# Optimization experiments

Hardware: AMD Instinct MI355X
Metric: run time of the kernel (lower is better)

Reference implementation:

```python
import jax, jax.numpy as jnp
import numpy as np

N_NODES = 100000
D_IN, D_OUT = 1024, 512
B, K = 8192, 64


def setup_inputs() -> dict:
    key = jax.random.key(0)
    k1, k2, k3, k4, k5 = jax.random.split(key, 5)
    X = jax.random.normal(k1, (N_NODES, D_IN), dtype=jnp.float32)
    indices = jax.random.randint(k2, (B, K), 0, N_NODES)  # top-K PPR neighbor ids per batch node
    values = jax.random.uniform(k3, (B, K), dtype=jnp.float32)  # PPR weights
    W = jax.random.normal(k4, (D_IN, D_OUT), dtype=jnp.float32) / np.sqrt(D_IN)
    b = jax.random.normal(k5, (D_OUT,), dtype=jnp.float32)
    return {"X": X, "indices": indices, "values": values, "W": W, "b": b}


def reference(X, indices, values, W, b):
    # Sparse PPR branch. Original: encode only unique gathered rows, then
    # re-expand via inverse indices. Since the encoder is row-pointwise,
    # encoder(X[u_fwd])[u_bwd] == encoder(X)[indices]; we encode all nodes once
    # (n_nodes < B*K here) then gather -- identical math, jit-friendly.
    enc = X @ W + b                      # [N, d_out]
    gathered = enc[indices]              # [B, K, d_out]
    return jnp.einsum('bk,bkd->bd', values, gathered)  # weighted sum over K neighbors
```

## Files before the change

### kernel.cpp

```cpp
#include <hip/hip_runtime.h>

typedef unsigned short ushort_t;
typedef __bf16 bf16x8 __attribute__((ext_vector_type(8)));
typedef float f32x4 __attribute__((ext_vector_type(4)));

#define N_NODES 100000
#define M_PAD   100096
#define D_IN    1024
#define D_OUT   512
#define B_SZ    8192
#define K_NB    64

__device__ __forceinline__ ushort_t f2bf(float f) {
    unsigned int u = __builtin_bit_cast(unsigned int, f);
    u += 0x7FFFu + ((u >> 16) & 1u);
    return (ushort_t)(u >> 16);
}
__device__ __forceinline__ float bflo(unsigned d) {
    return __builtin_bit_cast(float, d << 16);
}
__device__ __forceinline__ float bfhi(unsigned d) {
    return __builtin_bit_cast(float, d & 0xFFFF0000u);
}

__device__ __forceinline__ void gload16(const ushort_t* g, ushort_t* l) {
    __builtin_amdgcn_global_load_lds(
        (const __attribute__((address_space(1))) void*)g,
        (__attribute__((address_space(3))) void*)l,
        16, 0, 0);
}

__device__ __forceinline__ bf16x8 pack8(float4 a, float4 b) {
    bf16x8 r;
    r[0] = (__bf16)a.x; r[1] = (__bf16)a.y;
    r[2] = (__bf16)a.z; r[3] = (__bf16)a.w;
    r[4] = (__bf16)b.x; r[5] = (__bf16)b.y;
    r[6] = (__bf16)b.z; r[7] = (__bf16)b.w;
    return r;
}

__global__ __launch_bounds__(256) void cast_w_kernel(
        const float* __restrict__ W, ushort_t* __restrict__ Wt) {
    int o = blockIdx.x * 256 + threadIdx.x;
    int n = o >> 10;
    int k = o & 1023;
    Wt[o] = f2bf(W[k * D_OUT + n]);
}

__global__ __launch_bounds__(256) void encode_gemm_kernel(
        const float* __restrict__ X, const ushort_t* __restrict__ Wt,
        const float* __restrict__ bias, ushort_t* __restrict__ Enc) {
    int bid = blockIdx.x;
    int logical = (bid & 7) * 391 + (bid >> 3);
    int m0 = (logical >> 2) * 128;
    int n0 = (logical & 3) * 128;

    int tid = threadIdx.x;
    int lane = tid & 63;
    int wave = tid >> 6;
    int wm = (wave >> 1) * 64;
    int wn = (wave & 1) * 64;
    int quad = lane >> 4;
    int l16  = lane & 15;

    __shared__ __align__(16) ushort_t As[2 * 4096];
    __shared__ __align__(16) ushort_t Bs[2 * 4096];

    f32x4 acc[4][4];
    f32x4 zero = {0.f, 0.f, 0.f, 0.f};
    #pragma unroll
    for (int i = 0; i < 4; i++)
        #pragma unroll
        for (int j = 0; j < 4; j++)
            acc[i][j] = zero;

    int srow = tid >> 2;
    int kch  = tid & 3;
    int schk = kch ^ ((srow >> 2) & 3);

    const ushort_t* gb = Wt + (size_t)(n0 + srow) * D_IN + schk * 8;
    ushort_t* lb = Bs + tid * 8;
    const size_t rowskip = (size_t)64 * D_IN;

    int ar0 = m0 + srow;
    int ar1 = m0 + srow + 64;
    if (ar0 > N_NODES - 1) ar0 = N_NODES - 1;
    if (ar1 > N_NODES - 1) ar1 = N_NODES - 1;
    const float* pa0 = X + (size_t)ar0 * D_IN + kch * 8;
    const float* pa1 = X + (size_t)ar1 * D_IN + kch * 8;
    ushort_t* aw = As + srow * 32 + schk * 8;

    int rsw  = (l16 >> 2) & 3;
    int rchk = quad ^ rsw;

    {
        float4 f00 = *(const float4*)(pa0);
        float4 f01 = *(const float4*)(pa0 + 4);
        float4 f10 = *(const float4*)(pa1);
        float4 f11 = *(const float4*)(pa1 + 4);
        gload16(gb,           lb);
        gload16(gb + rowskip, lb + 2048);
        *(bf16x8*)(aw)           = pack8(f00, f01);
        *(bf16x8*)(aw + 64 * 32) = pack8(f10, f11);
    }
    __syncthreads();

    for (int it = 0; it < 32; ++it) {
        int p  = (it & 1) * 4096;
        int q  = 4096 - p;
        int k1 = it * 32 + 32;

        float4 g00, g01, g10, g11;
        bool has_next = (k1 < D_IN);
        if (has_next) {
            g00 = *(const float4*)(pa0 + k1);
            g01 = *(const float4*)(pa0 + k1 + 4);
            g10 = *(const float4*)(pa1 + k1);
            g11 = *(const float4*)(pa1 + k1 + 4);
            gload16(gb + k1,           lb + q);
            gload16(gb + rowskip + k1, lb + q + 2048);
        }

        bf16x8 a[4], b[4];
        #pragma unroll
        for (int i = 0; i < 4; i++) {
            a[i] = *(const bf16x8*)(As + p + (wm + i * 16 + l16) * 32 + rchk * 8);
            b[i] = *(const bf16x8*)(Bs + p + (wn + i * 16 + l16) * 32 + rchk * 8);
        }
        #pragma unroll
        for (int i = 0; i < 4; i++)
            #pragma unroll
            for (int j = 0; j < 4; j++)
                acc[i][j] = __builtin_amdgcn_mfma_f32_16x16x32_bf16(
                                a[i], b[j], acc[i][j], 0, 0, 0);

        if (has_next) {
            *(bf16x8*)(aw + q)           = pack8(g00, g01);
            *(bf16x8*)(aw + q + 64 * 32) = pack8(g10, g11);
        }
        __syncthreads();
    }

    float bv[4];
    #pragma unroll
    for (int j = 0; j < 4; j++) bv[j] = bias[n0 + wn + j * 16 + l16];

    #pragma unroll
    for (int i = 0; i < 4; i++) {
        #pragma unroll
        for (int r = 0; r < 4; r++) {
            int grow = m0 + wm + i * 16 + quad * 4 + r;
            if (grow < N_NODES) {
                #pragma unroll
                for (int j = 0; j < 4; j++) {
                    int gcol = n0 + wn + j * 16 + l16;
                    Enc[(size_t)grow * D_OUT + gcol] = f2bf(acc[i][j][r] + bv[j]);
                }
            }
        }
    }
}

__global__ __launch_bounds__(256) void gather_out_kernel(
        const ushort_t* __restrict__ Enc, const int* __restrict__ idx,
        const float* __restrict__ val, float* __restrict__ out) {
    int b = blockIdx.x;
    int t = threadIdx.x;

    __shared__ int   sidx[K_NB];
    __shared__ float sval[K_NB];
    __shared__ float part[8 * 3 * 64];
    if (t < K_NB) {
        sidx[t] = idx[b * K_NB + t];
        sval[t] = val[b * K_NB + t];
    }
    __syncthreads();

    int h = t >> 6;
    int c = t & 63;

    float acc[8] = {0.f, 0.f, 0.f, 0.f, 0.f, 0.f, 0.f, 0.f};

    uint4 x[8];
    #pragma unroll
    for (int u = 0; u < 8; u++)
        x[u] = ((const uint4*)(Enc + (size_t)sidx[h + 4 * u] * D_OUT))[c];

    #pragma unroll
    for (int j0 = 0; j0 < 16; j0 += 8) {
        uint4 cur[8];
        #pragma unroll
        for (int u = 0; u < 8; u++) cur[u] = x[u];
        if (j0 + 8 < 16) {
            #pragma unroll
            for (int u = 0; u < 8; u++)
                x[u] = ((const uint4*)(
                    Enc + (size_t)sidx[h + 4 * (j0 + 8 + u)] * D_OUT))[c];
        }
        #pragma unroll
        for (int u = 0; u < 8; u++) {
            float v = sval[h + 4 * (j0 + u)];
            acc[0] = fmaf(v, bflo(cur[u].x), acc[0]);
            acc[1] = fmaf(v, bfhi(cur[u].x), acc[1]);
            acc[2] = fmaf(v, bflo(cur[u].y), acc[2]);
            acc[3] = fmaf(v, bfhi(cur[u].y), acc[3]);
            acc[4] = fmaf(v, bflo(cur[u].z), acc[4]);
            acc[5] = fmaf(v, bfhi(cur[u].z), acc[5]);
            acc[6] = fmaf(v, bflo(cur[u].w), acc[6]);
            acc[7] = fmaf(v, bfhi(cur[u].w), acc[7]);
        }
    }

    if (h != 0) {
        #pragma unroll
        for (int e = 0; e < 8; e++)
            part[e * 192 + (h - 1) * 64 + c] = acc[e];
    }
    __syncthreads();
    if (h == 0) {
        float r[8];
        #pragma unroll
        for (int e = 0; e < 8; e++)
            r[e] = acc[e] + part[e * 192 + c] + part[e * 192 + 64 + c]
                          + part[e * 192 + 128 + c];
        float4 o0 = {r[0], r[1], r[2], r[3]};
        float4 o1 = {r[4], r[5], r[6], r[7]};
        float* dst = out + (size_t)b * D_OUT + c * 8;
        *(float4*)(dst)     = o0;
        *(float4*)(dst + 4) = o1;
    }
}

__global__ __launch_bounds__(256) void gather_f32_kernel(
        const float* __restrict__ X, const int* __restrict__ idx,
        const float* __restrict__ val, ushort_t* __restrict__ Y,
        float* __restrict__ s) {
    int b = blockIdx.x;
    int t = threadIdx.x;

    __shared__ int   sidx[K_NB];
    __shared__ float sval[K_NB];
    if (t < K_NB) {
        sidx[t] = idx[b * K_NB + t];
        sval[t] = val[b * K_NB + t];
    }
    __syncthreads();

    float ax = 0.f, ay = 0.f, az = 0.f, aw = 0.f;
    #pragma unroll 8
    for (int k = 0; k < K_NB; k++) {
        const float4* row = (const float4*)(X + (size_t)sidx[k] * D_IN);
        float4 x = row[t];
        float  v = sval[k];
        ax = fmaf(v, x.x, ax);
        ay = fmaf(v, x.y, ay);
        az = fmaf(v, x.z, az);
        aw = fmaf(v, x.w, aw);
    }
    uint2 o;
    o.x = (unsigned)f2bf(ax) | ((unsigned)f2bf(ay) << 16);
    o.y = (unsigned)f2bf(az) | ((unsigned)f2bf(aw) << 16);
    *(uint2*)(Y + (size_t)b * D_IN + t * 4) = o;

    if (t == 0) {
        float sum = 0.f;
        #pragma unroll
        for (int k = 0; k < K_NB; k++) sum += sval[k];
        s[b] = sum;
    }
}

__global__ __launch_bounds__(256) void gemm_kernel(
        const ushort_t* __restrict__ Y, const ushort_t* __restrict__ Wt,
        const float* __restrict__ s, const float* __restrict__ bias,
        float* __restrict__ out) {
    const int Kdim = D_IN;
    int m0 = blockIdx.x * 128;
    int n0 = blockIdx.y * 128;
    int t = threadIdx.x;
    int lane = t & 63;
    int wave = t >> 6;
    int wm = (wave >> 1) * 64;
    int wn = (wave & 1) * 64;
    int quad = lane >> 4;
    int l16  = lane & 15;

    __shared__ __align__(16) ushort_t As[128 * 32];
    __shared__ __align__(16) ushort_t Bs[128 * 32];

    f32x4 acc[4][4];
    f32x4 zero = {0.f, 0.f, 0.f, 0.f};
    #pragma unroll
    for (int i = 0; i < 4; i++)
        #pragma unroll
        for (int j = 0; j < 4; j++)
            acc[i][j] = zero;

    int rsw = (l16 >> 2) & 3;

    for (int k0 = 0; k0 < Kdim; k0 += 32) {
        #pragma unroll
        for (int i = 0; i < 2; i++) {
            int c   = t + i * 256;
            int row = c >> 2;
            int chk = c & 3;
            int pos = chk ^ ((row >> 2) & 3);
            *(int4*)(As + row * 32 + pos * 8) =
                *(const int4*)(Y + (size_t)(m0 + row) * Kdim + k0 + chk * 8);
            *(int4*)(Bs + row * 32 + pos * 8) =
                *(const int4*)(Wt + (size_t)(n0 + row) * Kdim + k0 + chk * 8);
        }
        __syncthreads();

        bf16x8 a[4], b[4];
        int rchk = quad ^ rsw;
        #pragma unroll
        for (int i = 0; i < 4; i++) {
            a[i] = *(const bf16x8*)(As + (wm + i * 16 + l16) * 32 + rchk * 8);
            b[i] = *(const bf16x8*)(Bs + (wn + i * 16 + l16) * 32 + rchk * 8);
        }
        #pragma unroll
        for (int i = 0; i < 4; i++)
            #pragma unroll
            for (int j = 0; j < 4; j++)
                acc[i][j] = __builtin_amdgcn_mfma_f32_16x16x32_bf16(
                                a[i], b[j], acc[i][j], 0, 0, 0);
        __syncthreads();
    }

    #pragma unroll
    for (int i = 0; i < 4; i++) {
        #pragma unroll
        for (int r = 0; r < 4; r++) {
            int grow = m0 + wm + i * 16 + quad * 4 + r;
            float sv = s[grow];
            #pragma unroll
            for (int j = 0; j < 4; j++) {
                int gcol = n0 + wn + j * 16 + l16;
                out[(size_t)grow * D_OUT + gcol] = acc[i][j][r] + sv * bias[gcol];
            }
        }
    }
}

extern "C" void kernel_launch(void* const* d_in, const int* in_sizes, int n_in,
                              void* d_out, int out_size, void* d_ws, size_t ws_size,
                              hipStream_t stream) {
    const float* X    = (const float*)d_in[0];
    const int*   idx  = (const int*)d_in[1];
    const float* val  = (const float*)d_in[2];
    const float* W    = (const float*)d_in[3];
    const float* bias = (const float*)d_in[4];
    float* out = (float*)d_out;

    const size_t ENC_BYTES = (size_t)M_PAD * D_OUT * 2;
    const size_t WT_BYTES  = (size_t)D_OUT * D_IN * 2;
    const size_t Y_BYTES   = (size_t)B_SZ * D_IN * 2;

    char* ws = (char*)d_ws;
    bool fast = ws_size >= ENC_BYTES + WT_BYTES;

    if (fast) {
        ushort_t* Enc = (ushort_t*)ws;
        ushort_t* Wt  = (ushort_t*)(ws + ENC_BYTES);

        hipLaunchKernelGGL(cast_w_kernel, dim3((D_OUT * D_IN) / 256), dim3(256),
                           0, stream, W, Wt);
        hipLaunchKernelGGL(encode_gemm_kernel, dim3((M_PAD / 128) * (D_OUT / 128)),
                           dim3(256), 0, stream, X, Wt, bias, Enc);
        hipLaunchKernelGGL(gather_out_kernel, dim3(B_SZ), dim3(256),
                           0, stream, Enc, idx, val, out);
    } else {
        ushort_t* Yb = (ushort_t*)ws;
        ushort_t* Wt = (ushort_t*)(ws + Y_BYTES);
        float*    sb = (float*)(ws + Y_BYTES + WT_BYTES);

        hipLaunchKernelGGL(cast_w_kernel, dim3((D_OUT * D_IN) / 256), dim3(256),
                           0, stream, W, Wt);
        hipLaunchKernelGGL(gather_f32_kernel, dim3(B_SZ), dim3(256),
                           0, stream, X, idx, val, Yb, sb);
        hipLaunchKernelGGL(gemm_kernel, dim3(B_SZ / 128, D_OUT / 128), dim3(256),
                           0, stream, Yb, Wt, sb, bias, out);
    }
}
```

Before: 783.9 us.

## Use single-buffered 64-wide K tiles with register prefetch in encode GEMM

The encode GEMM now steps through K in tiles of 64 instead of 32. It drops the LDS double buffer and uses one 128x64 tile per operand with an 8-chunk XOR swizzle. The next X tile is prefetched into registers while the MFMAs run on the current one. This halves the number of loop iterations and barriers and gives each barrier interval more MFMA work. The cost is that the W async loads are no longer overlapped with compute, since there are two barriers per iteration on a single buffer.

```diff
diff --git a/kernel.cpp b/kernel.cpp
--- a/kernel.cpp
+++ b/kernel.cpp
@@ -63,8 +63,8 @@
     int quad = lane >> 4;
     int l16  = lane & 15;
 
-    __shared__ __align__(16) ushort_t As[2 * 4096];
-    __shared__ __align__(16) ushort_t Bs[2 * 4096];
+    __shared__ __align__(16) ushort_t As[128 * 64];
+    __shared__ __align__(16) ushort_t Bs[128 * 64];
 
     f32x4 acc[4][4];
     f32x4 zero = {0.f, 0.f, 0.f, 0.f};
@@ -74,69 +74,63 @@
         for (int j = 0; j < 4; j++)
             acc[i][j] = zero;
 
-    int srow = tid >> 2;
-    int kch  = tid & 3;
-    int schk = kch ^ ((srow >> 2) & 3);
-
-    const ushort_t* gb = Wt + (size_t)(n0 + srow) * D_IN + schk * 8;
+    int rb  = tid >> 3;
+    int kc  = tid & 7;
+    int skc = kc ^ (rb & 7);
+
+    const ushort_t* gb = Wt + (size_t)(n0 + rb) * D_IN + skc * 8;
     ushort_t* lb = Bs + tid * 8;
-    const size_t rowskip = (size_t)64 * D_IN;
-
-    int ar0 = m0 + srow;
-    int ar1 = m0 + srow + 64;
-    if (ar0 > N_NODES - 1) ar0 = N_NODES - 1;
-    if (ar1 > N_NODES - 1) ar1 = N_NODES - 1;
-    const float* pa0 = X + (size_t)ar0 * D_IN + kch * 8;
-    const float* pa1 = X + (size_t)ar1 * D_IN + kch * 8;
-    ushort_t* aw = As + srow * 32 + schk * 8;
-
-    int rsw  = (l16 >> 2) & 3;
-    int rchk = quad ^ rsw;
-
-    {
-        float4 f00 = *(const float4*)(pa0);
-        float4 f01 = *(const float4*)(pa0 + 4);
-        float4 f10 = *(const float4*)(pa1);
-        float4 f11 = *(const float4*)(pa1 + 4);
-        gload16(gb,           lb);
-        gload16(gb + rowskip, lb + 2048);
-        *(bf16x8*)(aw)           = pack8(f00, f01);
-        *(bf16x8*)(aw + 64 * 32) = pack8(f10, f11);
-    }
-    __syncthreads();
-
-    for (int it = 0; it < 32; ++it) {
-        int p  = (it & 1) * 4096;
-        int q  = 4096 - p;
-        int k1 = it * 32 + 32;
-
-        float4 g00, g01, g10, g11;
-        bool has_next = (k1 < D_IN);
-        if (has_next) {
-            g00 = *(const float4*)(pa0 + k1);
-            g01 = *(const float4*)(pa0 + k1 + 4);
-            g10 = *(const float4*)(pa1 + k1);
-            g11 = *(const float4*)(pa1 + k1 + 4);
-            gload16(gb + k1,           lb + q);
-            gload16(gb + rowskip + k1, lb + q + 2048);
-        }
-
-        bf16x8 a[4], b[4];
-        #pragma unroll
-        for (int i = 0; i < 4; i++) {
-            a[i] = *(const bf16x8*)(As + p + (wm + i * 16 + l16) * 32 + rchk * 8);
-            b[i] = *(const bf16x8*)(Bs + p + (wn + i * 16 + l16) * 32 + rchk * 8);
-        }
+
+    const float* pa[4];
+    #pragma unroll
+    for (int i = 0; i < 4; i++) {
+        int r = m0 + rb + 32 * i;
+        if (r > N_NODES - 1) r = N_NODES - 1;
+        pa[i] = X + (size_t)r * D_IN + kc * 8;
+    }
+    ushort_t* aw = As + rb * 64 + skc * 8;
+
+    int rsw = l16 & 7;
+
+    float4 f[4][2];
+    #pragma unroll
+    for (int i = 0; i < 4; i++) {
+        f[i][0] = *(const float4*)(pa[i]);
+        f[i][1] = *(const float4*)(pa[i] + 4);
+    }
+
+    for (int k0 = 0; k0 < D_IN; k0 += 64) {
         #pragma unroll
         for (int i = 0; i < 4; i++)
-            #pragma unroll
-            for (int j = 0; j < 4; j++)
-                acc[i][j] = __builtin_amdgcn_mfma_f32_16x16x32_bf16(
-                                a[i], b[j], acc[i][j], 0, 0, 0);
-
-        if (has_next) {
-            *(bf16x8*)(aw + q)           = pack8(g00, g01);
-            *(bf16x8*)(aw + q + 64 * 32) = pack8(g10, g11);
+            *(bf16x8*)(aw + i * 2048) = pack8(f[i][0], f[i][1]);
+        #pragma unroll
+        for (int i = 0; i < 4; i++)
+            gload16(gb + k0 + (size_t)i * 32 * D_IN, lb + i * 2048);
+        __syncthreads();
+
+        if (k0 + 64 < D_IN) {
+            #pragma unroll
+            for (int i = 0; i < 4; i++) {
+                f[i][0] = *(const float4*)(pa[i] + k0 + 64);
+                f[i][1] = *(const float4*)(pa[i] + k0 + 68);
+            }
+        }
+
+        #pragma unroll
+        for (int s = 0; s < 2; s++) {
+            bf16x8 a[4], b[4];
+            int pos = ((s * 4 + quad) ^ rsw) * 8;
+            #pragma unroll
+            for (int i = 0; i < 4; i++) {
+                a[i] = *(const bf16x8*)(As + (wm + i * 16 + l16) * 64 + pos);
+                b[i] = *(const bf16x8*)(Bs + (wn + i * 16 + l16) * 64 + pos);
+            }
+            #pragma unroll
+            for (int i = 0; i < 4; i++)
+                #pragma unroll
+                for (int j = 0; j < 4; j++)
+                    acc[i][j] = __builtin_amdgcn_mfma_f32_16x16x32_bf16(
+                                    a[i], b[j], acc[i][j], 0, 0, 0);
         }
         __syncthreads();
     }
```

New measurement: 725.2 us. -7.5%, faster.
